# Optimization experiments

Hardware: AMD Instinct MI355X
Metric: run time of the kernel (lower is better)

## Reference

```python
import jax, jax.numpy as jnp
import numpy as np


def setup_inputs() -> dict:
    key = jax.random.key(0)
    k1, k2, k3 = jax.random.split(key, 3)
    B, N = 1024, 4096
    kp3d = jax.random.normal(k1, (B, N, 3), dtype=jnp.float32)
    ref_points = jax.random.uniform(k2, (B, N, 2), dtype=jnp.float32)
    weight = jax.random.uniform(k3, (B, N), dtype=jnp.float32)
    return {"kp3d": kp3d, "ref_points": ref_points, "weight": weight}


def reference(kp3d, ref_points, weight):
    # Projected 2D coords (perspective output already applied upstream).
    x = (kp3d[:, :, 0] + 1.0) * 0.5          # [B, N]
    y = 1.0 - (kp3d[:, :, 1] + 1.0) * 0.5    # [B, N]
    z = kp3d[:, :, 2]                         # [B, N]

    # my_normalize: per-batch-row min-max normalization (vectorized).
    # NOTE: result is computed but unused by the loss, exactly as in the
    # original forward (z = my_normalize(z) is dead afterwards).
    z_min = jnp.min(z, axis=1, keepdims=True)
    z_max = jnp.max(z, axis=1, keepdims=True)
    z_norm = (z - z_min) / (z_max - z_min)    # [B, N]

    kp2d = jnp.stack((x, y), axis=2)          # [B, N, 2]

    # kp_loss: weighted per-point 2D Euclidean distance, summed.
    diff = kp2d - ref_points                  # [B, N, 2]
    dist = jnp.sqrt(jnp.sum(diff * diff, axis=2))  # [B, N]
    loss = jnp.sum(weight * dist)
    # z_norm is dead code in the original; loss is the sole output.
    return loss
```

## Files before the change

### kernel.cpp

```cpp
#include <hip/hip_runtime.h>


#define TPB 256

__global__ __launch_bounds__(TPB) void viewpoint_partial_kernel(
    const float* __restrict__ kp3d,
    const float* __restrict__ ref,
    const float* __restrict__ w,
    float* __restrict__ partials,
    int T)
{
    const float4* kp4 = (const float4*)kp3d;
    const float4* rf4 = (const float4*)ref;
    const float4* w4  = (const float4*)w;

    int tid = blockIdx.x * TPB + threadIdx.x;
    int g0 = tid;
    int g1 = tid + T;

    float4 a0 = kp4[3 * g0 + 0];
    float4 a1 = kp4[3 * g0 + 1];
    float4 a2 = kp4[3 * g0 + 2];
    float4 b0 = kp4[3 * g1 + 0];
    float4 b1 = kp4[3 * g1 + 1];
    float4 b2 = kp4[3 * g1 + 2];
    float4 r00 = rf4[2 * g0 + 0];
    float4 r01 = rf4[2 * g0 + 1];
    float4 r10 = rf4[2 * g1 + 0];
    float4 r11 = rf4[2 * g1 + 1];
    float4 w0 = w4[g0];
    float4 w1 = w4[g1];

    float acc = 0.0f;
    float dx, dy;

    dx = fmaf(a0.x, 0.5f, 0.5f) - r00.x;
    dy = fmaf(a0.y, -0.5f, 0.5f) - r00.y;
    acc += w0.x * sqrtf(fmaf(dx, dx, dy * dy));

    dx = fmaf(a0.w, 0.5f, 0.5f) - r00.z;
    dy = fmaf(a1.x, -0.5f, 0.5f) - r00.w;
    acc += w0.y * sqrtf(fmaf(dx, dx, dy * dy));

    dx = fmaf(a1.z, 0.5f, 0.5f) - r01.x;
    dy = fmaf(a1.w, -0.5f, 0.5f) - r01.y;
    acc += w0.z * sqrtf(fmaf(dx, dx, dy * dy));

    dx = fmaf(a2.y, 0.5f, 0.5f) - r01.z;
    dy = fmaf(a2.z, -0.5f, 0.5f) - r01.w;
    acc += w0.w * sqrtf(fmaf(dx, dx, dy * dy));

    dx = fmaf(b0.x, 0.5f, 0.5f) - r10.x;
    dy = fmaf(b0.y, -0.5f, 0.5f) - r10.y;
    acc += w1.x * sqrtf(fmaf(dx, dx, dy * dy));

    dx = fmaf(b0.w, 0.5f, 0.5f) - r10.z;
    dy = fmaf(b1.x, -0.5f, 0.5f) - r10.w;
    acc += w1.y * sqrtf(fmaf(dx, dx, dy * dy));

    dx = fmaf(b1.z, 0.5f, 0.5f) - r11.x;
    dy = fmaf(b1.w, -0.5f, 0.5f) - r11.y;
    acc += w1.z * sqrtf(fmaf(dx, dx, dy * dy));

    dx = fmaf(b2.y, 0.5f, 0.5f) - r11.z;
    dy = fmaf(b2.z, -0.5f, 0.5f) - r11.w;
    acc += w1.w * sqrtf(fmaf(dx, dx, dy * dy));

    #pragma unroll
    for (int off = 32; off > 0; off >>= 1)
        acc += __shfl_down(acc, off, 64);

    __shared__ float wave_sums[TPB / 64];
    int lane = threadIdx.x & 63;
    int wid  = threadIdx.x >> 6;
    if (lane == 0) wave_sums[wid] = acc;
    __syncthreads();

    if (threadIdx.x == 0) {
        partials[blockIdx.x] = wave_sums[0] + wave_sums[1]
                             + wave_sums[2] + wave_sums[3];
    }
}

__global__ __launch_bounds__(256) void final_reduce_kernel(
    const float* __restrict__ partials, float* __restrict__ out, int n)
{
    float acc = 0.0f;
    for (int i = threadIdx.x; i < n; i += 256)
        acc += partials[i];

    #pragma unroll
    for (int off = 32; off > 0; off >>= 1)
        acc += __shfl_down(acc, off, 64);

    __shared__ float wave_sums[4];
    int lane = threadIdx.x & 63;
    int wid  = threadIdx.x >> 6;
    if (lane == 0) wave_sums[wid] = acc;
    __syncthreads();

    if (threadIdx.x == 0)
        out[0] = wave_sums[0] + wave_sums[1] + wave_sums[2] + wave_sums[3];
}

extern "C" void kernel_launch(void* const* d_in, const int* in_sizes, int n_in,
                              void* d_out, int out_size, void* d_ws, size_t ws_size,
                              hipStream_t stream) {
    const float* kp3d = (const float*)d_in[0];
    const float* ref  = (const float*)d_in[1];
    const float* w    = (const float*)d_in[2];
    float* out = (float*)d_out;
    float* partials = (float*)d_ws;

    int npts = in_sizes[2];
    int ngroups = npts / 4;
    int T = ngroups / 2;
    int blocks = T / TPB;

    viewpoint_partial_kernel<<<blocks, TPB, 0, stream>>>(kp3d, ref, w, partials, T);
    final_reduce_kernel<<<1, 256, 0, stream>>>(partials, out, blocks);
}
```

Baseline: 117.9 us.

## Stage coalesced loads through LDS and process one group per thread

Each block now loads its contiguous chunk of kp3d and ref_points into shared memory with fully coalesced float4 loads, then each thread reads its strided 3- and 2-float4 group from LDS. Work per thread drops from two point groups to one, which doubles the block count and the number of partial sums. This targets the strided global access pattern of the old per-thread loads, at the cost of an LDS round trip, a barrier, and less memory-level parallelism per thread.

```diff
diff --git a/kernel.cpp b/kernel.cpp
--- a/kernel.cpp
+++ b/kernel.cpp
@@ -7,64 +7,55 @@
     const float* __restrict__ kp3d,
     const float* __restrict__ ref,
     const float* __restrict__ w,
-    float* __restrict__ partials,
-    int T)
+    float* __restrict__ partials)
 {
     const float4* kp4 = (const float4*)kp3d;
     const float4* rf4 = (const float4*)ref;
     const float4* w4  = (const float4*)w;
 
-    int tid = blockIdx.x * TPB + threadIdx.x;
-    int g0 = tid;
-    int g1 = tid + T;
+    __shared__ float4 s_kp[TPB * 3];
+    __shared__ float4 s_rf[TPB * 2];
 
-    float4 a0 = kp4[3 * g0 + 0];
-    float4 a1 = kp4[3 * g0 + 1];
-    float4 a2 = kp4[3 * g0 + 2];
-    float4 b0 = kp4[3 * g1 + 0];
-    float4 b1 = kp4[3 * g1 + 1];
-    float4 b2 = kp4[3 * g1 + 2];
-    float4 r00 = rf4[2 * g0 + 0];
-    float4 r01 = rf4[2 * g0 + 1];
-    float4 r10 = rf4[2 * g1 + 0];
-    float4 r11 = rf4[2 * g1 + 1];
-    float4 w0 = w4[g0];
-    float4 w1 = w4[g1];
+    int t = threadIdx.x;
+    size_t blk = blockIdx.x;
+
+    size_t kb = blk * (TPB * 3);
+    size_t rb = blk * (TPB * 2);
+
+    float4 wv = w4[blk * TPB + t];
+
+    s_kp[t]            = kp4[kb + t];
+    s_kp[TPB + t]      = kp4[kb + TPB + t];
+    s_kp[2 * TPB + t]  = kp4[kb + 2 * TPB + t];
+    s_rf[t]            = rf4[rb + t];
+    s_rf[TPB + t]      = rf4[rb + TPB + t];
+
+    __syncthreads();
+
+    float4 a0 = s_kp[3 * t + 0];
+    float4 a1 = s_kp[3 * t + 1];
+    float4 a2 = s_kp[3 * t + 2];
+    float4 r0 = s_rf[2 * t + 0];
+    float4 r1 = s_rf[2 * t + 1];
 
     float acc = 0.0f;
     float dx, dy;
 
-    dx = fmaf(a0.x, 0.5f, 0.5f) - r00.x;
-    dy = fmaf(a0.y, -0.5f, 0.5f) - r00.y;
-    acc += w0.x * sqrtf(fmaf(dx, dx, dy * dy));
+    dx = fmaf(a0.x, 0.5f, 0.5f) - r0.x;
+    dy = fmaf(a0.y, -0.5f, 0.5f) - r0.y;
+    acc += wv.x * sqrtf(fmaf(dx, dx, dy * dy));
 
-    dx = fmaf(a0.w, 0.5f, 0.5f) - r00.z;
-    dy = fmaf(a1.x, -0.5f, 0.5f) - r00.w;
-    acc += w0.y * sqrtf(fmaf(dx, dx, dy * dy));
+    dx = fmaf(a0.w, 0.5f, 0.5f) - r0.z;
+    dy = fmaf(a1.x, -0.5f, 0.5f) - r0.w;
+    acc += wv.y * sqrtf(fmaf(dx, dx, dy * dy));
 
-    dx = fmaf(a1.z, 0.5f, 0.5f) - r01.x;
-    dy = fmaf(a1.w, -0.5f, 0.5f) - r01.y;
-    acc += w0.z * sqrtf(fmaf(dx, dx, dy * dy));
+    dx = fmaf(a1.z, 0.5f, 0.5f) - r1.x;
+    dy = fmaf(a1.w, -0.5f, 0.5f) - r1.y;
+    acc += wv.z * sqrtf(fmaf(dx, dx, dy * dy));
 
-    dx = fmaf(a2.y, 0.5f, 0.5f) - r01.z;
-    dy = fmaf(a2.z, -0.5f, 0.5f) - r01.w;
-    acc += w0.w * sqrtf(fmaf(dx, dx, dy * dy));
-
-    dx = fmaf(b0.x, 0.5f, 0.5f) - r10.x;
-    dy = fmaf(b0.y, -0.5f, 0.5f) - r10.y;
-    acc += w1.x * sqrtf(fmaf(dx, dx, dy * dy));
-
-    dx = fmaf(b0.w, 0.5f, 0.5f) - r10.z;
-    dy = fmaf(b1.x, -0.5f, 0.5f) - r10.w;
-    acc += w1.y * sqrtf(fmaf(dx, dx, dy * dy));
-
-    dx = fmaf(b1.z, 0.5f, 0.5f) - r11.x;
-    dy = fmaf(b1.w, -0.5f, 0.5f) - r11.y;
-    acc += w1.z * sqrtf(fmaf(dx, dx, dy * dy));
-
-    dx = fmaf(b2.y, 0.5f, 0.5f) - r11.z;
-    dy = fmaf(b2.z, -0.5f, 0.5f) - r11.w;
-    acc += w1.w * sqrtf(fmaf(dx, dx, dy * dy));
+    dx = fmaf(a2.y, 0.5f, 0.5f) - r1.z;
+    dy = fmaf(a2.z, -0.5f, 0.5f) - r1.w;
+    acc += wv.w * sqrtf(fmaf(dx, dx, dy * dy));
 
     #pragma unroll
     for (int off = 32; off > 0; off >>= 1)
@@ -113,10 +104,8 @@
     float* partials = (float*)d_ws;
 
     int npts = in_sizes[2];
-    int ngroups = npts / 4;
-    int T = ngroups / 2;
-    int blocks = T / TPB;
+    int blocks = npts / (TPB * 4);
 
-    viewpoint_partial_kernel<<<blocks, TPB, 0, stream>>>(kp3d, ref, w, partials, T);
+    viewpoint_partial_kernel<<<blocks, TPB, 0, stream>>>(kp3d, ref, w, partials);
     final_reduce_kernel<<<1, 256, 0, stream>>>(partials, out, blocks);
 }
```

Result: no change. 118.6 us, median of 2 (+0.7%).
